# Performance work log

Hardware: AMD Instinct MI355X
Metric: run time of the kernel (lower is better)

## Reference

```python
import jax, jax.numpy as jnp
import numpy as np

N_ROOMS = 300
N = N_ROOMS + 2          # state dim: 2 envelope nodes + rooms
M = N_ROOMS + 1          # input dim: [Tout; Q per room]
T = 60000                # number of t_eval points
DT = 30.0                # seconds between solution points
N_KNOTS = 2001           # Tout interpolation knots
ONE_THIRD = 1.0 / 3.0


def setup_inputs() -> dict:
    key = jax.random.key(0)
    k1, k2, k3, k4 = jax.random.split(key, 4)
    n_params = N * N + N_ROOMS
    params = jax.random.uniform(k1, (n_params,), jnp.float32)
    theta_lo = jnp.zeros((n_params,), jnp.float32)
    # conductance-like entries kept tiny so RK4 with h=30s stays stable
    theta_hi = jnp.concatenate([
        jnp.full((N * N,), 1e-4, jnp.float32),
        jnp.ones((N_ROOMS,), jnp.float32),
    ])
    B = jax.random.normal(k2, (N, M), jnp.float32) * 1e-3  # constant input matrix
    tout_t = jnp.linspace(0.0, T * DT, N_KNOTS).astype(jnp.float32)
    tout_vals = 15.0 + 10.0 * jax.random.normal(k3, (N_KNOTS,), jnp.float32)
    iv = 15.0 + 10.0 * jax.random.uniform(k4, (N, 1), jnp.float32)
    t_eval = jnp.arange(T, dtype=jnp.float32) * DT
    return {"params": params, "theta_lo": theta_lo, "theta_hi": theta_hi,
            "B": B, "tout_t": tout_t, "tout_vals": tout_vals,
            "iv": iv, "t_eval": t_eval, "t0": 0}


def reference(params, theta_lo, theta_hi, B, tout_t, tout_vals, iv, t_eval, t0):
    # transform + physical scaling of raw parameters
    x = jax.nn.sigmoid(params)
    theta = theta_lo + (theta_hi - theta_lo) * x
    W = theta[: N * N].reshape(N, N)
    # RC conductance matrix: diagonally dominant, negative diagonal (stable)
    A = W - jnp.diag(jnp.abs(W).sum(axis=1))
    Q = theta[N * N:]  # per-room heat gains [N_ROOMS]

    def f(t, y):
        # dy/dt = A y + B u,  u = [Tout(t + t0); Q]
        Tout = jnp.interp(t + t0, tout_t, tout_vals)
        u = jnp.concatenate([Tout[None], Q])[:, None]  # [M, 1]
        return A @ y + B @ u

    def step(y, th):
        # torchdiffeq method='rk4' uses the 3/8-rule (rk4_alt_step_func)
        t, h = th
        k1 = f(t, y)
        k2 = f(t + h * ONE_THIRD, y + h * ONE_THIRD * k1)
        k3 = f(t + 2.0 * h * ONE_THIRD, y + h * (k2 - ONE_THIRD * k1))
        k4 = f(t + h, y + h * (k1 - k2 + k3))
        y1 = y + (k1 + 3.0 * (k2 + k3) + k4) * (h * 0.125)
        return y1, y1

    ts = t_eval[:-1]
    hs = t_eval[1:] - t_eval[:-1]
    _, ys = jax.lax.scan(step, iv, (ts, hs))
    return jnp.concatenate([iv[None], ys], axis=0)  # [T, N, 1]
```

## Files before the change

### kernel.cpp

```cpp
#include <hip/hip_runtime.h>
#include <math.h>

#define NN     302
#define MM     301
#define NROOMS 300
#define NP     320
#define TS     59999
#define KN     2001
#define DTH    30.0f

#define L_CHUNK 128
#define N_CHUNK 469
#define N_WG2   235
#define N_BND   468
#define NB_PAD  480
#define N_GRP   30
#define NSCAN   29

#define WS_M    0
#define WS_M2   102400
#define WS_P    204800
#define WS_UV   307200
#define WS_B0C  308800
#define WS_TAU  309440
#define WS_W    549440
#define WS_G    754240
#define WS_Y    907840
#define WS_Z    1057920
#define WS_SA   1067520
#define WS_SB   1144320
#define WS_PL   1182720
#define WS_PA   1285120
#define WS_PB   1387520
#define WS_PT   1489920
#define WS_MT   2718720

typedef float vf2 __attribute__((ext_vector_type(2)));

#define ENGINE_LO __launch_bounds__(512) __attribute__((amdgpu_waves_per_eu(2, 2)))
#define PKFMA(acc, a, b) asm("v_pk_fma_f32 %0, %1, %2, %0" : "+v"(acc) : "v"(a), "v"(b))
#define PIN4(a, b, c, d) asm volatile("" : "+v"(a), "+v"(b), "+v"(c), "+v"(d))

__global__ __launch_bounds__(320) void phaseA_kernel(
    const float* __restrict__ params, const float* __restrict__ tlo,
    const float* __restrict__ thi, const float* __restrict__ B,
    const float* __restrict__ tout_t, const float* __restrict__ tout_v,
    const int* __restrict__ t0p,
    float* __restrict__ M, float* __restrict__ MT,
    float* __restrict__ b0c, float4* __restrict__ tau)
{
    __shared__ float red[5];
    __shared__ float Qs[NROOMS];
    const int b = blockIdx.x;
    const int tid = threadIdx.x;

    if (b < 320) {
        const int r = b;
        const int c = tid;
        float wv = 0.0f;
        if (r < NN && c < NN) {
            const int idx = r * NN + c;
            const float x = 1.0f / (1.0f + expf(-params[idx]));
            wv = tlo[idx] + (thi[idx] - tlo[idx]) * x;
        }
        float s = fabsf(wv);
        #pragma unroll
        for (int off = 32; off > 0; off >>= 1) s += __shfl_xor(s, off, 64);
        if ((c & 63) == 0) red[c >> 6] = s;
        __syncthreads();
        const float rs = red[0] + red[1] + red[2] + red[3] + red[4];
        float v = DTH * wv;
        if (r == c) v -= DTH * rs;
        M[r * NP + c] = v;
        MT[(size_t)c * NP + r] = v;
    } else if (b < 384) {
        for (int q = tid; q < NROOMS; q += 320) {
            const int idx = NN * NN + q;
            const float x = 1.0f / (1.0f + expf(-params[idx]));
            Qs[q] = tlo[idx] + (thi[idx] - tlo[idx]) * x;
        }
        __syncthreads();
        const int w = tid >> 6, l = tid & 63;
        const int r = (b - 320) * 5 + w;
        if (r >= NN) {
            if (l == 0) { b0c[r] = 0.0f; b0c[NP + r] = 0.0f; }
            return;
        }
        float s = 0.0f;
        for (int q = l; q < NROOMS; q += 64) s = fmaf(B[r * MM + 1 + q], Qs[q], s);
        #pragma unroll
        for (int off = 32; off > 0; off >>= 1) s += __shfl_xor(s, off, 64);
        if (l == 0) { b0c[r] = B[r * MM]; b0c[NP + r] = s; }
    } else {
        if (tid >= 256) return;
        const int n = (b - 384) * 256 + tid;
        if (n >= TS) return;
        const float tbase = 30.0f * (float)n + (float)(*t0p);
        float r[4];
        #pragma unroll
        for (int st = 0; st < 4; ++st) {
            const float x = tbase + 10.0f * (float)st;
            float res;
            if (x <= tout_t[0])            res = tout_v[0];
            else if (x >= tout_t[KN - 1])  res = tout_v[KN - 1];
            else {
                int k = (int)(x * (1.0f / 900.0f));
                if (k > KN - 2) k = KN - 2;
                if (k < 0) k = 0;
                if (x < tout_t[k] && k > 0) --k;
                else if (x >= tout_t[k + 1] && k < KN - 2) ++k;
                const float tk = tout_t[k], tk1 = tout_t[k + 1];
                const float wgt = (x - tk) / (tk1 - tk);
                res = tout_v[k] + wgt * (tout_v[k + 1] - tout_v[k]);
            }
            r[st] = res;
        }
        tau[n] = make_float4(r[0], r[1], r[2], r[3]);
    }
}

__global__ __launch_bounds__(320) void mm4r_vec_kernel(
    const float* __restrict__ A, float* __restrict__ C,
    const float* __restrict__ MT, const float* __restrict__ b0c,
    float* __restrict__ uv, const float* __restrict__ iv,
    float* __restrict__ W, float* __restrict__ out)
{
    const int b = blockIdx.x;
    const int tid = threadIdx.x;
    if (b < 80) {
        const int c = tid;
        const int r0 = b * 4;
        const float* Ar = A + (size_t)r0 * NP;
        float a0 = 0.f, a1 = 0.f, a2 = 0.f, a3 = 0.f;
        #pragma unroll 8
        for (int k = 0; k < NP; ++k) {
            const float bb = A[(size_t)k * NP + c];
            a0 = fmaf(Ar[k], bb, a0);
            a1 = fmaf(Ar[NP + k], bb, a1);
            a2 = fmaf(Ar[2 * NP + k], bb, a2);
            a3 = fmaf(Ar[3 * NP + k], bb, a3);
        }
        C[(size_t)r0 * NP + c] = a0;
        C[(size_t)(r0 + 1) * NP + c] = a1;
        C[(size_t)(r0 + 2) * NP + c] = a2;
        C[(size_t)(r0 + 3) * NP + c] = a3;
        return;
    }
    __shared__ float ysB[NP], ysC[NP];
    const float s = DTH / 8.0f;
    const float b0 = b0c[tid];
    const float cc = b0c[NP + tid];
    ysB[tid] = b0; ysC[tid] = cc;
    __syncthreads();

    float mb, mc, m2b, m2c, m3b, m3c;
    {
        float aB = 0.f, aC = 0.f;
        #pragma unroll 8
        for (int k = 0; k < NP; ++k) {
            const float a = MT[(size_t)k * NP + tid];
            aB = fmaf(a, ysB[k], aB);
            aC = fmaf(a, ysC[k], aC);
        }
        mb = aB; mc = aC;
    }
    __syncthreads(); ysB[tid] = mb; ysC[tid] = mc; __syncthreads();
    {
        float aB = 0.f, aC = 0.f;
        #pragma unroll 8
        for (int k = 0; k < NP; ++k) {
            const float a = MT[(size_t)k * NP + tid];
            aB = fmaf(a, ysB[k], aB);
            aC = fmaf(a, ysC[k], aC);
        }
        m2b = aB; m2c = aC;
    }
    __syncthreads(); ysB[tid] = m2b; ysC[tid] = m2c; __syncthreads();
    {
        float aB = 0.f, aC = 0.f;
        #pragma unroll 8
        for (int k = 0; k < NP; ++k) {
            const float a = MT[(size_t)k * NP + tid];
            aB = fmaf(a, ysB[k], aB);
            aC = fmaf(a, ysC[k], aC);
        }
        m3b = aB; m3c = aC;
    }

    const float u1 = s * (b0 + mb + (1.0f / 3.0f) * (m2b + m3b));
    const float u2 = s * (3.0f * b0 + 2.0f * mb + m2b);
    const float u3 = s * (3.0f * b0 + mb);
    const float u4 = s * b0;
    const float dd = s * (8.0f * cc + 4.0f * mc + (4.0f / 3.0f) * m2c + (1.0f / 3.0f) * m3c);

    uv[tid]          = u1;
    uv[NP + tid]     = u2;
    uv[2 * NP + tid] = u3;
    uv[3 * NP + tid] = u4;
    uv[4 * NP + tid] = dd;

    W[(size_t)(0 << 7) * NP + tid] = dd;
    W[(size_t)(1 << 7) * NP + tid] = u1;
    W[(size_t)(2 << 7) * NP + tid] = u2;
    W[(size_t)(3 << 7) * NP + tid] = u3;
    W[(size_t)(4 << 7) * NP + tid] = u4;

    if (tid < NN) out[tid] = iv[tid];
}

__global__ void matmulP(const float* __restrict__ M2, const float* __restrict__ M,
                        float* __restrict__ P, float* __restrict__ PT0)
{
    const int c = blockIdx.x * 64 + threadIdx.x;
    const int r0 = blockIdx.y * 4;
    const float* Ar = M2 + (size_t)r0 * NP;
    float a0 = 0.f, a1 = 0.f, a2 = 0.f, a3 = 0.f;
    #pragma unroll 8
    for (int k = 0; k < NP; ++k) {
        const size_t o = (size_t)k * NP + c;
        const float b = (1.0f / 6.0f) * M[o] + (1.0f / 24.0f) * M2[o];
        a0 = fmaf(Ar[k], b, a0);
        a1 = fmaf(Ar[NP + k], b, a1);
        a2 = fmaf(Ar[2 * NP + k], b, a2);
        a3 = fmaf(Ar[3 * NP + k], b, a3);
    }
    float acc[4] = {a0, a1, a2, a3};
    float4 t;
    #pragma unroll
    for (int u = 0; u < 4; ++u) {
        const int r = r0 + u;
        const size_t idx = (size_t)r * NP + c;
        float v = acc[u] + M[idx] + 0.5f * M2[idx];
        if (r == c && r < NN) v += 1.0f;
        P[idx] = v;
        ((float*)&t)[u] = v;
    }
    *(float4*)(PT0 + (size_t)c * NP + r0) = t;
}

__global__ __launch_bounds__(320) void fat_kernel(
    const float* __restrict__ src, float* __restrict__ dst,
    float* __restrict__ PTall, int j, float* __restrict__ W,
    const float* __restrict__ Sin, float* __restrict__ Sout, int npairs)
{
    const int b = blockIdx.x;
    const int tid = threadIdx.x;
    if (b < 320) {
        const int w = tid >> 6, l = tid & 63;
        const int r = (b & 63) * 5 + w;
        const int c = (b >> 6) * 64 + l;
        const float* Ar = src + (size_t)r * NP;
        float c0 = 0.f, c1 = 0.f, c2 = 0.f, c3 = 0.f;
        #pragma unroll 4
        for (int k = 0; k < NP; k += 4) {
            c0 = fmaf(Ar[k],     src[(size_t)k * NP + c],       c0);
            c1 = fmaf(Ar[k + 1], src[(size_t)(k + 1) * NP + c], c1);
            c2 = fmaf(Ar[k + 2], src[(size_t)(k + 2) * NP + c], c2);
            c3 = fmaf(Ar[k + 3], src[(size_t)(k + 3) * NP + c], c3);
        }
        const float acc = (c0 + c1) + (c2 + c3);
        dst[(size_t)r * NP + c] = acc;
        PTall[(size_t)(j + 1) * NP * NP + (size_t)c * NP + r] = acc;
        return;
    }
    const float* PTj = PTall + (size_t)j * NP * NP;
    const int c0 = (b - 320) * 4;
    __shared__ float ys[4][NP];
    if (j < 7) {
        const int nc = 5 << j;
        #pragma unroll
        for (int u = 0; u < 4; ++u) {
            const int ci = c0 + u;
            float val = 0.0f;
            if (ci < nc) {
                const int v = ci >> j, mo = ci & ((1 << j) - 1);
                val = W[(size_t)((v << 7) + mo) * NP + tid];
            }
            ys[u][tid] = val;
        }
        __syncthreads();
        float a0 = 0.f, a1 = 0.f, a2 = 0.f, a3 = 0.f;
        #pragma unroll 8
        for (int k = 0; k < NP; ++k) {
            const float p = PTj[(size_t)k * NP + tid];
            a0 = fmaf(p, ys[0][k], a0);
            a1 = fmaf(p, ys[1][k], a1);
            a2 = fmaf(p, ys[2][k], a2);
            a3 = fmaf(p, ys[3][k], a3);
        }
        const float acc[4] = {a0, a1, a2, a3};
        #pragma unroll
        for (int u = 0; u < 4; ++u) {
            const int ci = c0 + u;
            if (ci < nc) {
                const int v = ci >> j, mo = ci & ((1 << j) - 1);
                W[(size_t)((v << 7) + (1 << j) + mo) * NP + tid] = acc[u];
            }
        }
    } else {
        #pragma unroll
        for (int u = 0; u < 4; ++u) {
            const int k = c0 + u;
            ys[u][tid] = (k < npairs) ? Sin[(size_t)(2 * k) * NP + tid] : 0.0f;
        }
        __syncthreads();
        float a0 = 0.f, a1 = 0.f, a2 = 0.f, a3 = 0.f;
        #pragma unroll 8
        for (int k = 0; k < NP; ++k) {
            const float p = PTj[(size_t)k * NP + tid];
            a0 = fmaf(p, ys[0][k], a0);
            a1 = fmaf(p, ys[1][k], a1);
            a2 = fmaf(p, ys[2][k], a2);
            a3 = fmaf(p, ys[3][k], a3);
        }
        const float acc[4] = {a0, a1, a2, a3};
        #pragma unroll
        for (int u = 0; u < 4; ++u) {
            const int k = c0 + u;
            if (k < npairs)
                Sout[(size_t)k * NP + tid] = acc[u] + Sin[(size_t)(2 * k + 1) * NP + tid];
        }
    }
}

__global__ void gsum_kernel(const float* __restrict__ W,
                            const float4* __restrict__ tau,
                            float* __restrict__ G)
{
    const int r = blockIdx.x * 64 + threadIdx.x;
    const int c0 = blockIdx.y * 4;
    const float* W0 = W;
    const float* W1 = W + 1 * (size_t)L_CHUNK * NP;
    const float* W2 = W + 2 * (size_t)L_CHUNK * NP;
    const float* W3 = W + 3 * (size_t)L_CHUNK * NP;
    const float* W4 = W + 4 * (size_t)L_CHUNK * NP;
    const int cc0 = (c0     < N_BND) ? c0     : N_BND - 1;
    const int cc1 = (c0 + 1 < N_BND) ? c0 + 1 : N_BND - 1;
    const int cc2 = (c0 + 2 < N_BND) ? c0 + 2 : N_BND - 1;
    const int cc3 = (c0 + 3 < N_BND) ? c0 + 3 : N_BND - 1;
    const int nb0 = cc0 * L_CHUNK + L_CHUNK - 1;
    const int nb1 = cc1 * L_CHUNK + L_CHUNK - 1;
    const int nb2 = cc2 * L_CHUNK + L_CHUNK - 1;
    const int nb3 = cc3 * L_CHUNK + L_CHUNK - 1;
    float g0 = 0.f, g1 = 0.f, g2 = 0.f, g3 = 0.f;
    #pragma unroll 2
    for (int m = 0; m < L_CHUNK; ++m) {
        const float4 a0 = tau[nb0 - m];
        const float4 a1 = tau[nb1 - m];
        const float4 a2 = tau[nb2 - m];
        const float4 a3 = tau[nb3 - m];
        const size_t o = (size_t)m * NP + r;
        const float w0 = W0[o], w1 = W1[o], w2 = W2[o], w3 = W3[o], w4 = W4[o];
        float t;
        t = w0; t = fmaf(a0.x, w1, t); t = fmaf(a0.y, w2, t);
        t = fmaf(a0.z, w3, t); t = fmaf(a0.w, w4, t); g0 += t;
        t = w0; t = fmaf(a1.x, w1, t); t = fmaf(a1.y, w2, t);
        t = fmaf(a1.z, w3, t); t = fmaf(a1.w, w4, t); g1 += t;
        t = w0; t = fmaf(a2.x, w1, t); t = fmaf(a2.y, w2, t);
        t = fmaf(a2.z, w3, t); t = fmaf(a2.w, w4, t); g2 += t;
        t = w0; t = fmaf(a3.x, w1, t); t = fmaf(a3.y, w2, t);
        t = fmaf(a3.z, w3, t); t = fmaf(a3.w, w4, t); g3 += t;
    }
    G[(size_t)(c0    ) * NP + r] = (c0     < N_BND) ? g0 : 0.f;
    G[(size_t)(c0 + 1) * NP + r] = (c0 + 1 < N_BND) ? g1 : 0.f;
    G[(size_t)(c0 + 2) * NP + r] = (c0 + 2 < N_BND) ? g2 : 0.f;
    G[(size_t)(c0 + 3) * NP + r] = (c0 + 3 < N_BND) ? g3 : 0.f;
}

__device__ __forceinline__ void load_pfrag(const float* __restrict__ Psrc,
                                           vf2 p[5][20], int l, int w)
{
    #pragma unroll
    for (int k = 0; k < 5; ++k) {
        const int row = (k < 4) ? (4 * l + k) : (256 + l);
        const float* Pr = Psrc + (size_t)row * NP + 40 * w;
        #pragma unroll
        for (int j4 = 0; j4 < 10; ++j4) {
            const float4 v4 = *(const float4*)(Pr + 4 * j4);
            vf2 a; a.x = v4.x; a.y = v4.y;
            vf2 b; b.x = v4.z; b.y = v4.w;
            p[k][2 * j4] = a;
            p[k][2 * j4 + 1] = b;
        }
    }
    #pragma unroll
    for (int k = 0; k < 5; ++k)
        #pragma unroll
        for (int jj = 0; jj < 20; jj += 4)
            PIN4(p[k][jj], p[k][jj + 1], p[k][jj + 2], p[k][jj + 3]);
}

__device__ __forceinline__ void fma_phase(const vf2 p[5][20],
                                          const float* __restrict__ yb,
                                          float* __restrict__ pw, int l)
{
    vf2 a0 = {0.f, 0.f}, a1 = {0.f, 0.f}, a2 = {0.f, 0.f},
        a3 = {0.f, 0.f}, a4 = {0.f, 0.f};
    #pragma unroll
    for (int j4 = 0; j4 < 10; ++j4) {
        const float4 yv = *(const float4*)(yb + 4 * j4);
        vf2 y01; y01.x = yv.x; y01.y = yv.y;
        vf2 y23; y23.x = yv.z; y23.y = yv.w;
        const int jj = 2 * j4;
        PKFMA(a0, p[0][jj], y01); PKFMA(a0, p[0][jj + 1], y23);
        PKFMA(a1, p[1][jj], y01); PKFMA(a1, p[1][jj + 1], y23);
        PKFMA(a2, p[2][jj], y01); PKFMA(a2, p[2][jj + 1], y23);
        PKFMA(a3, p[3][jj], y01); PKFMA(a3, p[3][jj + 1], y23);
        PKFMA(a4, p[4][jj], y01); PKFMA(a4, p[4][jj + 1], y23);
    }
    float4 h4;
    h4.x = a0.x + a0.y;
    h4.y = a1.x + a1.y;
    h4.z = a2.x + a2.y;
    h4.w = a3.x + a3.y;
    *(float4*)(pw + 4 * l) = h4;
    pw[256 + l] = a4.x + a4.y;
}

__device__ __forceinline__ float reduce8(const float* __restrict__ pb, int r)
{
    float s = pb[r];
    #pragma unroll
    for (int k = 1; k < 8; ++k) s += pb[k * NP + r];
    return s;
}

__global__ ENGINE_LO void bscan_kernel(
    const float* __restrict__ PK, const float* __restrict__ S4,
    const float* __restrict__ iv, float* __restrict__ Z)
{
    const int tid = threadIdx.x;
    const int w = tid >> 6, l = tid & 63;
    vf2 p[5][20];
    load_pfrag(PK, p, l, w);

    __shared__ float ybuf[NP];
    __shared__ float part[2 * 8 * NP];
    __shared__ float ring[NSCAN * NP];

    const int r = 40 * w + l;
    if (tid < NP) {
        const float y0 = (tid < NN) ? iv[tid] : 0.f;
        ybuf[tid] = y0;
        Z[tid] = y0;
    }
    float sv = (l < 40) ? S4[r] : 0.f;
    __syncthreads();

    for (int g = 0; g < NSCAN; ++g) {
        float* pb = part + (g & 1) * 8 * NP;
        fma_phase(p, ybuf + 40 * w, pb + w * NP, l);
        const float svn = (l < 40 && g + 1 < NSCAN)
                        ? S4[(size_t)(g + 1) * NP + r] : 0.f;
        __syncthreads();
        if (l < 40) {
            const float yn = reduce8(pb, r) + sv;
            ybuf[r] = yn;
            ring[g * NP + r] = yn;
        }
        sv = svn;
    }
    __syncthreads();
    for (int s2 = 0; s2 < NSCAN; ++s2)
        for (int j = tid; j < NP; j += 512)
            Z[(size_t)(s2 + 1) * NP + j] = ring[s2 * NP + j];
}

__global__ ENGINE_LO void brefill_kernel(
    const float* __restrict__ PL, const float* __restrict__ G,
    const float* __restrict__ Z, float* __restrict__ Y)
{
    const int tid = threadIdx.x;
    const int w = tid >> 6, l = tid & 63;
    vf2 p[5][20];
    load_pfrag(PL, p, l, w);

    __shared__ float ybuf[NP];
    __shared__ float part[2 * 8 * NP];
    __shared__ float ring[16 * NP];

    const int g = blockIdx.x;
    const int nsteps = (16 * g + 16 <= N_BND) ? 16 : (N_BND - 16 * g);
    const int r = 40 * w + l;
    if (tid < NP) {
        const float z = Z[(size_t)g * NP + tid];
        ybuf[tid] = z;
        if (g == 0) Y[tid] = z;
    }
    float gv = (l < 40) ? G[(size_t)(16 * g) * NP + r] : 0.f;
    __syncthreads();

    for (int i = 0; i < nsteps; ++i) {
        float* pb = part + (i & 1) * 8 * NP;
        fma_phase(p, ybuf + 40 * w, pb + w * NP, l);
        const float gvn = (l < 40 && i + 1 < nsteps)
                        ? G[(size_t)(16 * g + i + 1) * NP + r] : 0.f;
        __syncthreads();
        if (l < 40) {
            const float yn = reduce8(pb, r) + gv;
            ybuf[r] = yn;
            ring[i * NP + r] = yn;
        }
        gv = gvn;
    }
    __syncthreads();
    for (int s2 = 0; s2 < nsteps; ++s2)
        for (int j = tid; j < NP; j += 512)
            Y[(size_t)(16 * g + 1 + s2) * NP + j] = ring[s2 * NP + j];
}

__global__ ENGINE_LO void refill_kernel(
    const float* __restrict__ P, const float* __restrict__ uv,
    const float4* __restrict__ tau, const float* __restrict__ Y,
    float* __restrict__ out)
{
    const int tid = threadIdx.x;
    const int w = tid >> 6, l = tid & 63;
    vf2 p[5][20];
    load_pfrag(P, p, l, w);

    __shared__ float ybufA[NP], ybufB[NP];
    __shared__ float partA[8 * NP], partB[8 * NP];
    __shared__ float ringA[8 * NP], ringB[8 * NP];
    __shared__ float4 tausA[8], tausB[8];

    const int r = 40 * w + l;
    float du0 = 0.f, du1 = 0.f, du2 = 0.f, du3 = 0.f, dd = 0.f;
    if (l < 40) {
        du0 = uv[r]; du1 = uv[NP + r]; du2 = uv[2 * NP + r];
        du3 = uv[3 * NP + r]; dd = uv[4 * NP + r];
    }

    const int b = blockIdx.x;
    const int cA = 2 * b, cB = 2 * b + 1;
    const int n0A = cA * L_CHUNK;
    const int n0B = cB * L_CHUNK;
    const int nA = (n0A + L_CHUNK < TS) ? L_CHUNK : (TS - n0A);
    const bool hasB = (cB < N_CHUNK);

    if (tid < NP) {
        ybufA[tid] = Y[(size_t)cA * NP + tid];
        if (hasB) ybufB[tid] = Y[(size_t)cB * NP + tid];
    }
    if (tid < 8) {
        if (tid < nA) tausA[tid] = tau[n0A + tid];
        if (hasB) tausB[tid] = tau[n0B + tid];
    }
    int wsA = 0, wsB = 0;
    __syncthreads();

    for (int i = 0; i < nA; ++i) {
        if (i - wsA == 8) {
            #pragma unroll 1
            for (int s2 = 0; s2 < 8; ++s2) {
                const size_t row = (size_t)(n0A + wsA + 1 + s2);
                for (int j = tid; j < NN; j += 512)
                    out[row * NN + j] = ringA[s2 * NP + j];
            }
            wsA = i;
            if (tid < 8 && i + tid < nA) tausA[tid] = tau[n0A + i + tid];
        }
        fma_phase(p, ybufA + 40 * w, partA + w * NP, l);
        if (hasB && i > 0) {
            const int sb = (i - 1) - wsB;
            const float4 a = tausB[sb];
            if (l < 40) {
                float yn = reduce8(partB, r) + dd;
                yn = fmaf(a.x, du0, yn);
                yn = fmaf(a.y, du1, yn);
                yn = fmaf(a.z, du2, yn);
                yn = fmaf(a.w, du3, yn);
                ybufB[r] = yn;
                ringB[sb * NP + r] = yn;
            }
        }
        __syncthreads();
        if (hasB && i - wsB == 8) {
            #pragma unroll 1
            for (int s2 = 0; s2 < 8; ++s2) {
                const size_t row = (size_t)(n0B + wsB + 1 + s2);
                for (int j = tid; j < NN; j += 512)
                    out[row * NN + j] = ringB[s2 * NP + j];
            }
            wsB = i;
            if (tid < 8) tausB[tid] = tau[n0B + i + tid];
        }
        if (hasB) fma_phase(p, ybufB + 40 * w, partB + w * NP, l);
        {
            const int sa = i - wsA;
            const float4 a = tausA[sa];
            if (l < 40) {
                float yn = reduce8(partA, r) + dd;
                yn = fmaf(a.x, du0, yn);
                yn = fmaf(a.y, du1, yn);
                yn = fmaf(a.z, du2, yn);
                yn = fmaf(a.w, du3, yn);
                ybufA[r] = yn;
                ringA[sa * NP + r] = yn;
            }
        }
        __syncthreads();
    }

    if (hasB) {
        const int sb = (nA - 1) - wsB;
        const float4 a = tausB[sb];
        if (l < 40) {
            float yn = reduce8(partB, r) + dd;
            yn = fmaf(a.x, du0, yn);
            yn = fmaf(a.y, du1, yn);
            yn = fmaf(a.z, du2, yn);
            yn = fmaf(a.w, du3, yn);
            ringB[sb * NP + r] = yn;
        }
    }
    __syncthreads();
    {
        const int cntA = nA - wsA;
        for (int s2 = 0; s2 < cntA; ++s2) {
            const size_t row = (size_t)(n0A + wsA + 1 + s2);
            for (int j = tid; j < NN; j += 512)
                out[row * NN + j] = ringA[s2 * NP + j];
        }
        if (hasB) {
            const int cntB = nA - wsB;
            for (int s2 = 0; s2 < cntB; ++s2) {
                const size_t row = (size_t)(n0B + wsB + 1 + s2);
                for (int j = tid; j < NN; j += 512)
                    out[row * NN + j] = ringB[s2 * NP + j];
            }
        }
    }
}

extern "C" void kernel_launch(void* const* d_in, const int* in_sizes, int n_in,
                              void* d_out, int out_size, void* d_ws, size_t ws_size,
                              hipStream_t stream)
{
    const float* params = (const float*)d_in[0];
    const float* tlo    = (const float*)d_in[1];
    const float* thi    = (const float*)d_in[2];
    const float* B      = (const float*)d_in[3];
    const float* tout_t = (const float*)d_in[4];
    const float* tout_v = (const float*)d_in[5];
    const float* iv     = (const float*)d_in[6];
    const int*   t0     = (const int*)d_in[8];
    float* out = (float*)d_out;
    float* ws  = (float*)d_ws;

    float*  M    = ws + WS_M;
    float*  MT   = ws + WS_MT;
    float*  M2   = ws + WS_M2;
    float*  P    = ws + WS_P;
    float*  UV   = ws + WS_UV;
    float*  B0C  = ws + WS_B0C;
    float4* TAU  = (float4*)(ws + WS_TAU);
    float*  W    = ws + WS_W;
    float*  G    = ws + WS_G;
    float*  Y    = ws + WS_Y;
    float*  Z    = ws + WS_Z;
    float*  SA   = ws + WS_SA;
    float*  SB   = ws + WS_SB;
    float*  PL   = ws + WS_PL;
    float*  PA   = ws + WS_PA;
    float*  PB   = ws + WS_PB;
    float*  PT   = ws + WS_PT;

    phaseA_kernel<<<619, 320, 0, stream>>>(params, tlo, thi, B, tout_t,
                                           tout_v, t0, M, MT, B0C, TAU);

    mm4r_vec_kernel<<<81, 320, 0, stream>>>(M, M2, MT, B0C, UV, iv, W, out);

    matmulP<<<dim3(5, 80), 64, 0, stream>>>(M2, M, P, PT);

    const float* src = P;
    for (int j = 0; j < 7; ++j) {
        float* dst = (j == 6) ? PL : ((j & 1) ? PB : PA);
        const int aux = ((5 << j) + 3) / 4;
        fat_kernel<<<320 + aux, 320, 0, stream>>>(src, dst, PT, j, W,
                                                  nullptr, nullptr, 0);
        src = dst;
    }
    gsum_kernel<<<dim3(5, NB_PAD / 4), 64, 0, stream>>>(W, TAU, G);
    const float* Spp[5] = { G, SA, SB, SA, SB };
    for (int j = 7; j < 11; ++j) {
        float* dst = (j & 1) ? PB : PA;
        const int npairs = 30720 >> j;
        const int aux = (npairs + 3) / 4;
        fat_kernel<<<320 + aux, 320, 0, stream>>>(src, dst, PT, j, W,
                                                  Spp[j - 7], (float*)Spp[j - 6], npairs);
        src = dst;
    }

    bscan_kernel<<<1, 512, 0, stream>>>(PA, SB, iv, Z);
    brefill_kernel<<<N_GRP, 512, 0, stream>>>(PL, G, Z, Y);

    refill_kernel<<<N_WG2, 512, 0, stream>>>(P, UV, TAU, Y, out);
}
```

Measured before the change: 689.3 us.

## Split refill matvec across 16 waves with 1024-thread workgroups

The refill kernel moves from 8 waves of 512 threads to 16 waves of 1024 threads. Each wave now holds half as many P columns in registers (20 instead of 40), and the partial sums are reduced over 16 slices instead of 8. The final reduction is spread over the first 320 threads instead of 40 lanes per wave. This halves the per-thread FMA chain on the serial step-to-step critical path and doubles the waves available to hide latency. In exchange it doubles the partial-sum shared memory and the length of the reduction, and it drops the waves-per-EU hint.

```diff
diff --git a/kernel.cpp b/kernel.cpp
--- a/kernel.cpp
+++ b/kernel.cpp
@@ -38,8 +38,10 @@
 typedef float vf2 __attribute__((ext_vector_type(2)));
 
 #define ENGINE_LO __launch_bounds__(512) __attribute__((amdgpu_waves_per_eu(2, 2)))
+#define ENGINE16  __launch_bounds__(1024)
 #define PKFMA(acc, a, b) asm("v_pk_fma_f32 %0, %1, %2, %0" : "+v"(acc) : "v"(a), "v"(b))
 #define PIN4(a, b, c, d) asm volatile("" : "+v"(a), "+v"(b), "+v"(c), "+v"(d))
+#define PIN2(a, b) asm volatile("" : "+v"(a), "+v"(b))
 
 __global__ __launch_bounds__(320) void phaseA_kernel(
     const float* __restrict__ params, const float* __restrict__ tlo,
@@ -425,6 +427,65 @@
     return s;
 }
 
+__device__ __forceinline__ void load_pfrag16(const float* __restrict__ Psrc,
+                                             vf2 p[5][10], int l, int w)
+{
+    #pragma unroll
+    for (int k = 0; k < 5; ++k) {
+        const int row = (k < 4) ? (4 * l + k) : (256 + l);
+        const float* Pr = Psrc + (size_t)row * NP + 20 * w;
+        #pragma unroll
+        for (int j4 = 0; j4 < 5; ++j4) {
+            const float4 v4 = *(const float4*)(Pr + 4 * j4);
+            vf2 a; a.x = v4.x; a.y = v4.y;
+            vf2 b; b.x = v4.z; b.y = v4.w;
+            p[k][2 * j4] = a;
+            p[k][2 * j4 + 1] = b;
+        }
+    }
+    #pragma unroll
+    for (int k = 0; k < 5; ++k) {
+        PIN4(p[k][0], p[k][1], p[k][2], p[k][3]);
+        PIN4(p[k][4], p[k][5], p[k][6], p[k][7]);
+        PIN2(p[k][8], p[k][9]);
+    }
+}
+
+__device__ __forceinline__ void fma_phase16(const vf2 p[5][10],
+                                            const float* __restrict__ yb,
+                                            float* __restrict__ pw, int l)
+{
+    vf2 a0 = {0.f, 0.f}, a1 = {0.f, 0.f}, a2 = {0.f, 0.f},
+        a3 = {0.f, 0.f}, a4 = {0.f, 0.f};
+    #pragma unroll
+    for (int j4 = 0; j4 < 5; ++j4) {
+        const float4 yv = *(const float4*)(yb + 4 * j4);
+        vf2 y01; y01.x = yv.x; y01.y = yv.y;
+        vf2 y23; y23.x = yv.z; y23.y = yv.w;
+        const int jj = 2 * j4;
+        PKFMA(a0, p[0][jj], y01); PKFMA(a0, p[0][jj + 1], y23);
+        PKFMA(a1, p[1][jj], y01); PKFMA(a1, p[1][jj + 1], y23);
+        PKFMA(a2, p[2][jj], y01); PKFMA(a2, p[2][jj + 1], y23);
+        PKFMA(a3, p[3][jj], y01); PKFMA(a3, p[3][jj + 1], y23);
+        PKFMA(a4, p[4][jj], y01); PKFMA(a4, p[4][jj + 1], y23);
+    }
+    float4 h4;
+    h4.x = a0.x + a0.y;
+    h4.y = a1.x + a1.y;
+    h4.z = a2.x + a2.y;
+    h4.w = a3.x + a3.y;
+    *(float4*)(pw + 4 * l) = h4;
+    pw[256 + l] = a4.x + a4.y;
+}
+
+__device__ __forceinline__ float reduce16(const float* __restrict__ pb, int r)
+{
+    float s = pb[r];
+    #pragma unroll
+    for (int k = 1; k < 16; ++k) s += pb[k * NP + r];
+    return s;
+}
+
 __global__ ENGINE_LO void bscan_kernel(
     const float* __restrict__ PK, const float* __restrict__ S4,
     const float* __restrict__ iv, float* __restrict__ Z)
@@ -509,26 +570,25 @@
             Y[(size_t)(16 * g + 1 + s2) * NP + j] = ring[s2 * NP + j];
 }
 
-__global__ ENGINE_LO void refill_kernel(
+__global__ ENGINE16 void refill_kernel(
     const float* __restrict__ P, const float* __restrict__ uv,
     const float4* __restrict__ tau, const float* __restrict__ Y,
     float* __restrict__ out)
 {
     const int tid = threadIdx.x;
     const int w = tid >> 6, l = tid & 63;
-    vf2 p[5][20];
-    load_pfrag(P, p, l, w);
+    vf2 p[5][10];
+    load_pfrag16(P, p, l, w);
 
     __shared__ float ybufA[NP], ybufB[NP];
-    __shared__ float partA[8 * NP], partB[8 * NP];
+    __shared__ __align__(16) float partA[16 * NP], partB[16 * NP];
     __shared__ float ringA[8 * NP], ringB[8 * NP];
     __shared__ float4 tausA[8], tausB[8];
 
-    const int r = 40 * w + l;
     float du0 = 0.f, du1 = 0.f, du2 = 0.f, du3 = 0.f, dd = 0.f;
-    if (l < 40) {
-        du0 = uv[r]; du1 = uv[NP + r]; du2 = uv[2 * NP + r];
-        du3 = uv[3 * NP + r]; dd = uv[4 * NP + r];
+    if (tid < NP) {
+        du0 = uv[tid]; du1 = uv[NP + tid]; du2 = uv[2 * NP + tid];
+        du3 = uv[3 * NP + tid]; dd = uv[4 * NP + tid];
     }
 
     const int b = blockIdx.x;
@@ -554,79 +614,73 @@
             #pragma unroll 1
             for (int s2 = 0; s2 < 8; ++s2) {
                 const size_t row = (size_t)(n0A + wsA + 1 + s2);
-                for (int j = tid; j < NN; j += 512)
+                for (int j = tid; j < NN; j += 1024)
                     out[row * NN + j] = ringA[s2 * NP + j];
             }
             wsA = i;
             if (tid < 8 && i + tid < nA) tausA[tid] = tau[n0A + i + tid];
         }
-        fma_phase(p, ybufA + 40 * w, partA + w * NP, l);
-        if (hasB && i > 0) {
+        fma_phase16(p, ybufA + 20 * w, partA + w * NP, l);
+        if (hasB && i > 0 && tid < NP) {
             const int sb = (i - 1) - wsB;
             const float4 a = tausB[sb];
-            if (l < 40) {
-                float yn = reduce8(partB, r) + dd;
-                yn = fmaf(a.x, du0, yn);
-                yn = fmaf(a.y, du1, yn);
-                yn = fmaf(a.z, du2, yn);
-                yn = fmaf(a.w, du3, yn);
-                ybufB[r] = yn;
-                ringB[sb * NP + r] = yn;
-            }
+            float yn = reduce16(partB, tid) + dd;
+            yn = fmaf(a.x, du0, yn);
+            yn = fmaf(a.y, du1, yn);
+            yn = fmaf(a.z, du2, yn);
+            yn = fmaf(a.w, du3, yn);
+            ybufB[tid] = yn;
+            ringB[sb * NP + tid] = yn;
         }
         __syncthreads();
         if (hasB && i - wsB == 8) {
             #pragma unroll 1
             for (int s2 = 0; s2 < 8; ++s2) {
                 const size_t row = (size_t)(n0B + wsB + 1 + s2);
-                for (int j = tid; j < NN; j += 512)
+                for (int j = tid; j < NN; j += 1024)
                     out[row * NN + j] = ringB[s2 * NP + j];
             }
             wsB = i;
             if (tid < 8) tausB[tid] = tau[n0B + i + tid];
         }
-        if (hasB) fma_phase(p, ybufB + 40 * w, partB + w * NP, l);
-        {
+        if (hasB) fma_phase16(p, ybufB + 20 * w, partB + w * NP, l);
+        if (tid < NP) {
             const int sa = i - wsA;
             const float4 a = tausA[sa];
-            if (l < 40) {
-                float yn = reduce8(partA, r) + dd;
-                yn = fmaf(a.x, du0, yn);
-                yn = fmaf(a.y, du1, yn);
-                yn = fmaf(a.z, du2, yn);
-                yn = fmaf(a.w, du3, yn);
-                ybufA[r] = yn;
-                ringA[sa * NP + r] = yn;
-            }
-        }
-        __syncthreads();
-    }
-
-    if (hasB) {
-        const int sb = (nA - 1) - wsB;
-        const float4 a = tausB[sb];
-        if (l < 40) {
-            float yn = reduce8(partB, r) + dd;
+            float yn = reduce16(partA, tid) + dd;
             yn = fmaf(a.x, du0, yn);
             yn = fmaf(a.y, du1, yn);
             yn = fmaf(a.z, du2, yn);
             yn = fmaf(a.w, du3, yn);
-            ringB[sb * NP + r] = yn;
-        }
+            ybufA[tid] = yn;
+            ringA[sa * NP + tid] = yn;
+        }
+        __syncthreads();
+    }
+
+    if (hasB && tid < NP) {
+        const int sb = (nA - 1) - wsB;
+        const float4 a = tausB[sb];
+        float yn = reduce16(partB, tid) + dd;
+        yn = fmaf(a.x, du0, yn);
+        yn = fmaf(a.y, du1, yn);
+        yn = fmaf(a.z, du2, yn);
+        yn = fmaf(a.w, du3, yn);
+        ringB[sb * NP + tid] = yn;
     }
     __syncthreads();
     {
         const int cntA = nA - wsA;
         for (int s2 = 0; s2 < cntA; ++s2) {
             const size_t row = (size_t)(n0A + wsA + 1 + s2);
-            for (int j = tid; j < NN; j += 512)
+            for (int j = tid; j < NN; j += 1024)
                 out[row * NN + j] = ringA[s2 * NP + j];
         }
         if (hasB) {
             const int cntB = nA - wsB;
             for (int s2 = 0; s2 < cntB; ++s2) {
                 const size_t row = (size_t)(n0B + wsB + 1 + s2);
-                for (int j = tid; j < NN; j += 512)
+                for (int j = tid; j < NN; j += 1024)
                     out[row * NN + j] = ringB[s2 * NP + j];
             }
         }
@@ -695,5 +749,5 @@
     bscan_kernel<<<1, 512, 0, stream>>>(PA, SB, iv, Z);
     brefill_kernel<<<N_GRP, 512, 0, stream>>>(PL, G, Z, Y);
 
-    refill_kernel<<<N_WG2, 512, 0, stream>>>(P, UV, TAU, Y, out);
-}
+    refill_kernel<<<N_WG2, 1024, 0, stream>>>(P, UV, TAU, Y, out);
+}
```

Result: slower. 957.6 us (+38.9%).

## Split matmul work across more blocks with split-K in the squaring kernel

Applied to the files above, without the earlier changes.

The 320x320 matrix products used to build the power chain are repartitioned to expose more parallelism. The M*M and P products now use one output row per block (320 blocks) instead of four rows per block. The repeated-squaring part of fat_kernel uses 640 blocks, each splitting K into two halves reduced through shared memory. The aim is to fill the MI355X's many compute units during these latency-bound serial matmul stages, at the cost of less register reuse of B loads, an extra barrier, and uncoalesced 32-wide column tiles.

```diff
diff --git a/kernel.cpp b/kernel.cpp
--- a/kernel.cpp
+++ b/kernel.cpp
@@ -127,23 +127,18 @@
 {
     const int b = blockIdx.x;
     const int tid = threadIdx.x;
-    if (b < 80) {
+    if (b < 320) {
         const int c = tid;
-        const int r0 = b * 4;
-        const float* Ar = A + (size_t)r0 * NP;
+        const float* Ar = A + (size_t)b * NP;
         float a0 = 0.f, a1 = 0.f, a2 = 0.f, a3 = 0.f;
-        #pragma unroll 8
-        for (int k = 0; k < NP; ++k) {
-            const float bb = A[(size_t)k * NP + c];
-            a0 = fmaf(Ar[k], bb, a0);
-            a1 = fmaf(Ar[NP + k], bb, a1);
-            a2 = fmaf(Ar[2 * NP + k], bb, a2);
-            a3 = fmaf(Ar[3 * NP + k], bb, a3);
-        }
-        C[(size_t)r0 * NP + c] = a0;
-        C[(size_t)(r0 + 1) * NP + c] = a1;
-        C[(size_t)(r0 + 2) * NP + c] = a2;
-        C[(size_t)(r0 + 3) * NP + c] = a3;
+        #pragma unroll 4
+        for (int k = 0; k < NP; k += 4) {
+            a0 = fmaf(Ar[k],     A[(size_t)k * NP + c],       a0);
+            a1 = fmaf(Ar[k + 1], A[(size_t)(k + 1) * NP + c], a1);
+            a2 = fmaf(Ar[k + 2], A[(size_t)(k + 2) * NP + c], a2);
+            a3 = fmaf(Ar[k + 3], A[(size_t)(k + 3) * NP + c], a3);
+        }
+        C[(size_t)b * NP + c] = (a0 + a1) + (a2 + a3);
         return;
     }
     __shared__ float ysB[NP], ysC[NP];
@@ -208,34 +203,27 @@
     if (tid < NN) out[tid] = iv[tid];
 }
 
-__global__ void matmulP(const float* __restrict__ M2, const float* __restrict__ M,
-                        float* __restrict__ P, float* __restrict__ PT0)
-{
-    const int c = blockIdx.x * 64 + threadIdx.x;
-    const int r0 = blockIdx.y * 4;
-    const float* Ar = M2 + (size_t)r0 * NP;
+__global__ __launch_bounds__(320) void matmulP(
+    const float* __restrict__ M2, const float* __restrict__ M,
+    float* __restrict__ P, float* __restrict__ PT0)
+{
+    const int c = threadIdx.x;
+    const int r = blockIdx.x;
+    const float* Ar = M2 + (size_t)r * NP;
     float a0 = 0.f, a1 = 0.f, a2 = 0.f, a3 = 0.f;
-    #pragma unroll 8
-    for (int k = 0; k < NP; ++k) {
+    #pragma unroll 4
+    for (int k = 0; k < NP; k += 4) {
         const size_t o = (size_t)k * NP + c;
-        const float b = (1.0f / 6.0f) * M[o] + (1.0f / 24.0f) * M2[o];
-        a0 = fmaf(Ar[k], b, a0);
-        a1 = fmaf(Ar[NP + k], b, a1);
-        a2 = fmaf(Ar[2 * NP + k], b, a2);
-        a3 = fmaf(Ar[3 * NP + k], b, a3);
-    }
-    float acc[4] = {a0, a1, a2, a3};
-    float4 t;
-    #pragma unroll
-    for (int u = 0; u < 4; ++u) {
-        const int r = r0 + u;
-        const size_t idx = (size_t)r * NP + c;
-        float v = acc[u] + M[idx] + 0.5f * M2[idx];
-        if (r == c && r < NN) v += 1.0f;
-        P[idx] = v;
-        ((float*)&t)[u] = v;
-    }
-    *(float4*)(PT0 + (size_t)c * NP + r0) = t;
+        a0 = fmaf(Ar[k],     (1.0f / 6.0f) * M[o]          + (1.0f / 24.0f) * M2[o],          a0);
+        a1 = fmaf(Ar[k + 1], (1.0f / 6.0f) * M[o + NP]     + (1.0f / 24.0f) * M2[o + NP],     a1);
+        a2 = fmaf(Ar[k + 2], (1.0f / 6.0f) * M[o + 2 * NP] + (1.0f / 24.0f) * M2[o + 2 * NP], a2);
+        a3 = fmaf(Ar[k + 3], (1.0f / 6.0f) * M[o + 3 * NP] + (1.0f / 24.0f) * M2[o + 3 * NP], a3);
+    }
+    const size_t idx = (size_t)r * NP + c;
+    float v = (a0 + a1) + (a2 + a3) + M[idx] + 0.5f * M2[idx];
+    if (r == c && r < NN) v += 1.0f;
+    P[idx] = v;
+    PT0[(size_t)c * NP + r] = v;
 }
 
 __global__ __launch_bounds__(320) void fat_kernel(
@@ -245,26 +233,36 @@
 {
     const int b = blockIdx.x;
     const int tid = threadIdx.x;
-    if (b < 320) {
-        const int w = tid >> 6, l = tid & 63;
-        const int r = (b & 63) * 5 + w;
-        const int c = (b >> 6) * 64 + l;
-        const float* Ar = src + (size_t)r * NP;
+    if (b < 640) {
+        __shared__ float psum[160];
+        const int half = tid / 160;
+        const int idx  = tid - half * 160;
+        const int rr = idx >> 5;
+        const int cc = idx & 31;
+        const int r = (b & 63) * 5 + rr;
+        const int c = (b >> 6) * 32 + cc;
+        const float* Ar = src + (size_t)r * NP + 160 * half;
+        const float* Bc = src + (size_t)(160 * half) * NP + c;
         float c0 = 0.f, c1 = 0.f, c2 = 0.f, c3 = 0.f;
         #pragma unroll 4
-        for (int k = 0; k < NP; k += 4) {
-            c0 = fmaf(Ar[k],     src[(size_t)k * NP + c],       c0);
-            c1 = fmaf(Ar[k + 1], src[(size_t)(k + 1) * NP + c], c1);
-            c2 = fmaf(Ar[k + 2], src[(size_t)(k + 2) * NP + c], c2);
-            c3 = fmaf(Ar[k + 3], src[(size_t)(k + 3) * NP + c], c3);
-        }
-        const float acc = (c0 + c1) + (c2 + c3);
-        dst[(size_t)r * NP + c] = acc;
-        PTall[(size_t)(j + 1) * NP * NP + (size_t)c * NP + r] = acc;
+        for (int k = 0; k < 160; k += 4) {
+            c0 = fmaf(Ar[k],     Bc[(size_t)k * NP],       c0);
+            c1 = fmaf(Ar[k + 1], Bc[(size_t)(k + 1) * NP], c1);
+            c2 = fmaf(Ar[k + 2], Bc[(size_t)(k + 2) * NP], c2);
+            c3 = fmaf(Ar[k + 3], Bc[(size_t)(k + 3) * NP], c3);
+        }
+        const float part = (c0 + c1) + (c2 + c3);
+        if (half == 1) psum[idx] = part;
+        __syncthreads();
+        if (half == 0) {
+            const float acc = part + psum[idx];
+            dst[(size_t)r * NP + c] = acc;
+            PTall[(size_t)(j + 1) * NP * NP + (size_t)c * NP + r] = acc;
+        }
         return;
     }
     const float* PTj = PTall + (size_t)j * NP * NP;
-    const int c0 = (b - 320) * 4;
+    const int c0 = (b - 640) * 4;
     __shared__ float ys[4][NP];
     if (j < 7) {
         const int nc = 5 << j;
@@ -669,15 +667,15 @@
     phaseA_kernel<<<619, 320, 0, stream>>>(params, tlo, thi, B, tout_t,
                                            tout_v, t0, M, MT, B0C, TAU);
 
-    mm4r_vec_kernel<<<81, 320, 0, stream>>>(M, M2, MT, B0C, UV, iv, W, out);
-
-    matmulP<<<dim3(5, 80), 64, 0, stream>>>(M2, M, P, PT);
+    mm4r_vec_kernel<<<321, 320, 0, stream>>>(M, M2, MT, B0C, UV, iv, W, out);
+
+    matmulP<<<320, 320, 0, stream>>>(M2, M, P, PT);
 
     const float* src = P;
     for (int j = 0; j < 7; ++j) {
         float* dst = (j == 6) ? PL : ((j & 1) ? PB : PA);
         const int aux = ((5 << j) + 3) / 4;
-        fat_kernel<<<320 + aux, 320, 0, stream>>>(src, dst, PT, j, W,
+        fat_kernel<<<640 + aux, 320, 0, stream>>>(src, dst, PT, j, W,
                                                   nullptr, nullptr, 0);
         src = dst;
     }
@@ -687,7 +685,7 @@
         float* dst = (j & 1) ? PB : PA;
         const int npairs = 30720 >> j;
         const int aux = (npairs + 3) / 4;
-        fat_kernel<<<320 + aux, 320, 0, stream>>>(src, dst, PT, j, W,
+        fat_kernel<<<640 + aux, 320, 0, stream>>>(src, dst, PT, j, W,
                                                   Spp[j - 7], (float*)Spp[j - 6], npairs);
         src = dst;
     }
```

After: 707.8 us. 1.03x slower.
